# Performance work log

Hardware: AMD Instinct MI355X
Metric: run time of the kernel (lower is better)

The kernel has to match this reference:

```python
import jax, jax.numpy as jnp
import numpy as np
from jax.scipy.linalg import expm
jax.config.update("jax_enable_x64", True)

HBAR = 0.6582119569
CM2EV = 0.00012398419
N6A, N10A = 4, 4
DT = 1.0
KDC = dict(E_S1=3.995, E_S2=4.9183, om6a=596.0 * CM2EV, om10a=919.0 * CM2EV,
           kap6a_S1=-0.0964, kap6a_S2=0.1193, lam=0.1825, gamma=-0.018)


def _build():
    cd = np.complex128

    def ladder(n):
        a = np.zeros((n, n), dtype=cd)
        for k in range(1, n):
            a[k - 1, k] = np.sqrt(float(k))
        adag = a.conj().T
        return (a + adag) / np.sqrt(2.0), adag @ a, np.eye(n, dtype=cd)

    Q6a1, N6a1, I6a = ladder(N6A)
    Q10a1, N10a1, I10a = ladder(N10A)
    Nel, Dvib = 3, N6A * N10A
    Ivib = np.eye(Dvib, dtype=cd)
    Iel = np.eye(Nel, dtype=cd)
    lift = lambda op: np.kron(Iel, op)
    Q6a = lift(np.kron(Q6a1, I10a))
    Q10a = lift(np.kron(I6a, Q10a1))
    N6a = lift(np.kron(N6a1, I10a))
    N10a = lift(np.kron(I6a, N10a1))
    P = []
    for k in range(Nel):
        ek = np.zeros(Nel, dtype=cd); ek[k] = 1.0
        P.append(np.kron(np.outer(ek, ek), Ivib))
    e1 = np.zeros(Nel, dtype=cd); e1[1] = 1.0
    e2 = np.zeros(Nel, dtype=cd); e2[2] = 1.0
    Poff = np.kron(np.outer(e1, e2) + np.outer(e2, e1), Ivib)
    Lj = np.kron(np.outer(e1, e2), Ivib)  # |S1><S2| lift
    D = Nel * Dvib
    I = np.eye(D, dtype=cd)
    p = KDC
    H = (p['E_S1'] * P[1] + p['E_S2'] * P[2] + p['om6a'] * N6a + p['om10a'] * N10a
         + p['kap6a_S1'] * P[1] @ Q6a + p['kap6a_S2'] * P[2] @ Q6a
         + p['lam'] * Poff @ Q10a + p['gamma'] * Poff @ (Q10a @ Q10a))
    # Coherent part -i(I kron H - H^T* kron I); dissipator at unit rate (scaled by g later)
    Lc = -1j * (np.kron(I, H) - np.kron(H.conj().T, I))
    LdL = Lj.conj().T @ Lj
    Ld0 = (np.kron(Lj.conj(), Lj) - 0.5 * np.kron(I, LdL)
           - 0.5 * np.kron(LdL.conj().T, I))
    psi = np.zeros(D, dtype=cd); psi[2 * N6A * N10A] = 1.0
    rho0 = np.outer(psi, psi.conj()).reshape(-1)
    trP = np.stack([P[k].T.reshape(-1) for k in range(3)])  # [3, D^2]
    return Lc, Ld0, rho0, trP

_LC, _LD0, _RHO0, _TRP = _build()


def setup_inputs() -> dict:
    return {"log_g": jnp.asarray(np.log(1.0 / 40.0), dtype=jnp.float32),
            "n_steps": 1000}


def reference(log_g, n_steps):
    Lc = jnp.asarray(_LC)
    Ld0 = jnp.asarray(_LD0)
    rho0 = jnp.asarray(_RHO0)
    trP = jnp.asarray(_TRP)
    g = jnp.exp(log_g).astype(jnp.float64)
    Lsup = Lc + g * Ld0                      # [D^2, D^2] complex128
    U = expm(Lsup * (DT / HBAR))             # one-step propagator

    def step(rho, _):
        pops = jnp.real(trP @ rho)           # tr(P_k rho), k=0..2
        return U @ rho, pops

    _, ps = jax.lax.scan(step, rho0, None, length=int(n_steps))  # [n_steps, 3]
    return (ps[:, 0].astype(jnp.float32),
            ps[:, 1].astype(jnp.float32),
            ps[:, 2].astype(jnp.float32))
```

## Files before the change

kernel.cpp:

```cpp
#include <hip/hip_runtime.h>
#include <math.h>


#define DS 1024
#define MATD ((size_t)DS * DS * sizeof(double))
#define PA 66

typedef double v4d __attribute__((ext_vector_type(4)));

__device__ inline double Qel(int i, int j) {
    if (i == j + 1) return sqrt((double)i) * 0.70710678118654752440;
    if (j == i + 1) return sqrt((double)j) * 0.70710678118654752440;
    return 0.0;
}

__device__ inline void fill_H(double* Hs, int tid) {
    const double CM2EV = 0.00012398419;
    const double E_S1 = 3.995, E_S2 = 4.9183;
    const double om6a = 596.0 * CM2EV, om10a = 919.0 * CM2EV;
    const double kapA = -0.0964, kapB = 0.1193, lam = 0.1825, gam = -0.018;
    for (int h = tid; h < 1024; h += 256) {
        int r = h >> 5, c = h & 31;
        int e = r >> 4, v6 = (r >> 2) & 3, v10 = r & 3;
        int e2 = c >> 4, w6 = (c >> 2) & 3, w10 = c & 3;
        double val = 0.0;
        if (r == c) val += (e ? E_S2 : E_S1) + om6a * v6 + om10a * v10;
        if (e == e2 && v10 == w10) val += (e ? kapB : kapA) * Qel(v6, w6);
        if (e != e2 && v6 == w6) {
            double q2 = 0.0;
            #pragma unroll
            for (int m = 0; m < 4; ++m) q2 += Qel(v10, m) * Qel(m, w10);
            val += lam * Qel(v10, w10) + gam * q2;
        }
        Hs[h] = val;
    }
}

__global__ __launch_bounds__(256)
void build_G14(const float* __restrict__ logg, double* __restrict__ X,
               double* __restrict__ Y, double* __restrict__ Z)
{
    int tid = threadIdx.x;
    if (blockIdx.x >= 4096) {
        int idx = (blockIdx.x - 4096) * 256 + tid;
        if (idx < 64 * 1024) {
            int r = idx >> 10, i = idx & 1023;
            double v = 0.0;
            if (r < 2 && i % 33 == 0) {
                int a = i / 33;
                if ((a < 16) == (r == 0)) v = 1.0;
            }
            Y[idx] = v;
        } else if (idx < 64 * 1024 + 1024) {
            int i = idx - 64 * 1024;
            Z[i] = (i == 528) ? 1.0 : 0.0;
        }
        return;
    }
    __shared__ double Hs[1024];
    fill_H(Hs, tid);
    __syncthreads();
    double g = exp((double)logg[0]);
    const double sc = ((1.0 / 0.6582119569) / 8.0) / 14.0;
    int idx = blockIdx.x * 256 + tid;
    int r = idx >> 10, c = idx & 1023;
    int i = r >> 5, j = r & 31;
    int k = c >> 5, l = c & 31;
    double t = 0.0;
    if (k <= l) {
        if (i <= j) {
            if (i < 16 && j < 16) {
                int p = i + 16, q = j + 16;
                if ((p == k && q == l) || (p == l && q == k)) t += g;
            }
            if (i == k && j == l) t -= 0.5 * g * ((i >= 16) + (j >= 16));
        } else {
            if (j == l) t += Hs[i * 32 + k];
            if (k != l && j == k) t += Hs[i * 32 + l];
            if (i == k) t -= Hs[l * 32 + j];
            if (k != l && i == l) t -= Hs[k * 32 + j];
        }
    } else {
        if (i <= j) {
            double ha = 0.0;
            if (j == l) ha += Hs[i * 32 + k];
            if (j == k) ha -= Hs[i * 32 + l];
            if (i == k) ha -= Hs[l * 32 + j];
            if (i == l) ha += Hs[k * 32 + j];
            t -= ha;
        } else {
            if (i < 16 && j < 16 && (i + 16 == k) && (j + 16 == l)) t += g;
            if (i == k && j == l) t -= 0.5 * g * ((i >= 16) + (j >= 16));
        }
    }
    X[idx] = t * sc + ((r == c) ? 1.0 : 0.0);
}

__global__ __launch_bounds__(256)
void apply_T(const float* __restrict__ logg, const double* __restrict__ M,
             double* __restrict__ O, double invk)
{
    __shared__ double Hs[1024];
    const int tid = threadIdx.x;
    fill_H(Hs, tid);
    __syncthreads();
    const double g = exp((double)logg[0]);
    const double sck = ((1.0 / 0.6582119569) / 8.0) * invk;
    const int p = ((blockIdx.x & 7) << 7) | (blockIdx.x >> 3);
    const int i = p >> 5, j = p & 31;

    double a0 = 0.0, a1 = 0.0, a2 = 0.0, a3 = 0.0;
    const int e = tid;

#define ADDROW(q, wgt) { const double* r_ = M + (size_t)(q) * DS; double w_ = (wgt); \
    a0 += w_ * r_[e]; a1 += w_ * r_[e + 256];                                        \
    a2 += w_ * r_[e + 512]; a3 += w_ * r_[e + 768]; }

    if (i <= j) {
        for (int m = 0; m < 32; ++m) {
            double c = Hs[i * 32 + m];
            if (c != 0.0 && m != j) {
                if (m > j) ADDROW(m * 32 + j, -c)
                else       ADDROW(j * 32 + m,  c)
            }
        }
        for (int m = 0; m < 32; ++m) {
            double c = Hs[m * 32 + j];
            if (c != 0.0 && m != i) {
                if (i > m) ADDROW(i * 32 + m,  c)
                else       ADDROW(m * 32 + i, -c)
            }
        }
        if (i < 16 && j < 16) ADDROW((i + 16) * 32 + (j + 16), g)
        if (i >= 16 || j >= 16)
            ADDROW(p, -0.5 * g * (double)((i >= 16) + (j >= 16)))
    } else {
        for (int m = 0; m < 32; ++m) {
            double c = Hs[i * 32 + m];
            if (c != 0.0) {
                int lo = m < j ? m : j, hi = m < j ? j : m;
                ADDROW(lo * 32 + hi, c)
            }
        }
        for (int m = 0; m < 32; ++m) {
            double c = Hs[m * 32 + j];
            if (c != 0.0) {
                int lo = m < i ? m : i, hi = m < i ? i : m;
                ADDROW(lo * 32 + hi, -c)
            }
        }
        if (i < 16 && j < 16) ADDROW((i + 16) * 32 + (j + 16), g)
        ADDROW(p, -0.5 * g * (double)((i >= 16) + (j >= 16)))
    }
#undef ADDROW

    size_t base = (size_t)p * DS;
    O[base + e]       = sck * a0 + ((p == e)       ? 1.0 : 0.0);
    O[base + e + 256] = sck * a1 + ((p == e + 256) ? 1.0 : 0.0);
    O[base + e + 512] = sck * a2 + ((p == e + 512) ? 1.0 : 0.0);
    O[base + e + 768] = sck * a3 + ((p == e + 768) ? 1.0 : 0.0);
}

__global__ __launch_bounds__(1024, 1)
void dgemm(const double* __restrict__ A, const double* __restrict__ B,
           double* __restrict__ D)
{
    __shared__ double As[2][64 * PA];
    __shared__ double Bs[2][64 * PA];
    const int tid = threadIdx.x;
    const int bm = blockIdx.x << 6, bn = blockIdx.y << 6;
    const int w = tid >> 6, lane = tid & 63;
    const int lr = lane & 15, lk = lane >> 4;
    const int p = w & 3, kg = w >> 2;
    const int wr = (p >> 1) << 5, wc = (p & 1) << 5;

    v4d acc[2][2];
    #pragma unroll
    for (int si = 0; si < 2; ++si)
        #pragma unroll
        for (int sj = 0; sj < 2; ++sj) acc[si][sj] = (v4d){0., 0., 0., 0.};

    const int ra = tid >> 4;
    const int cs = (tid & 15) << 2;
    const double* gA = A + (size_t)(bm + ra) * DS + cs;
    const double* gB = B + (size_t)ra * DS + bn + cs;
    double va[4], vb[4];
    #pragma unroll
    for (int u = 0; u < 4; ++u) { va[u] = gA[u]; vb[u] = gB[u]; }
    #pragma unroll
    for (int u = 0; u < 4; ++u) {
        As[0][ra * PA + cs + u] = va[u];
        Bs[0][ra * PA + cs + u] = vb[u];
    }
    __syncthreads();

    #pragma unroll 2
    for (int kt = 0; kt < DS; kt += 64) {
        const int pb = (kt >> 6) & 1;
        const bool more = (kt + 64) < DS;
        if (more) {
            #pragma unroll
            for (int u = 0; u < 4; ++u) {
                va[u] = gA[kt + 64 + u];
                vb[u] = gB[(size_t)(kt + 64) * DS + u];
            }
        }
        const int k0 = (kg << 4) + lk;
        double A00 = As[pb][(wr + lr) * PA + k0];
        double A10 = As[pb][(wr + 16 + lr) * PA + k0];
        double B00 = Bs[pb][k0 * PA + wc + lr];
        double B10 = Bs[pb][k0 * PA + wc + 16 + lr];
        double A01 = As[pb][(wr + lr) * PA + k0 + 4];
        double A11 = As[pb][(wr + 16 + lr) * PA + k0 + 4];
        double B01 = Bs[pb][(k0 + 4) * PA + wc + lr];
        double B11 = Bs[pb][(k0 + 4) * PA + wc + 16 + lr];
        acc[0][0] = __builtin_amdgcn_mfma_f64_16x16x4f64(A00, B00, acc[0][0], 0, 0, 0);
        acc[0][1] = __builtin_amdgcn_mfma_f64_16x16x4f64(A00, B10, acc[0][1], 0, 0, 0);
        acc[1][0] = __builtin_amdgcn_mfma_f64_16x16x4f64(A10, B00, acc[1][0], 0, 0, 0);
        acc[1][1] = __builtin_amdgcn_mfma_f64_16x16x4f64(A10, B10, acc[1][1], 0, 0, 0);
        acc[0][0] = __builtin_amdgcn_mfma_f64_16x16x4f64(A01, B01, acc[0][0], 0, 0, 0);
        acc[0][1] = __builtin_amdgcn_mfma_f64_16x16x4f64(A01, B11, acc[0][1], 0, 0, 0);
        acc[1][0] = __builtin_amdgcn_mfma_f64_16x16x4f64(A11, B01, acc[1][0], 0, 0, 0);
        acc[1][1] = __builtin_amdgcn_mfma_f64_16x16x4f64(A11, B11, acc[1][1], 0, 0, 0);
        if (more) {
            #pragma unroll
            for (int u = 0; u < 4; ++u) {
                As[pb ^ 1][ra * PA + cs + u] = va[u];
                Bs[pb ^ 1][ra * PA + cs + u] = vb[u];
            }
        }
        double A02 = As[pb][(wr + lr) * PA + k0 + 8];
        double A12 = As[pb][(wr + 16 + lr) * PA + k0 + 8];
        double B02 = Bs[pb][(k0 + 8) * PA + wc + lr];
        double B12 = Bs[pb][(k0 + 8) * PA + wc + 16 + lr];
        double A03 = As[pb][(wr + lr) * PA + k0 + 12];
        double A13 = As[pb][(wr + 16 + lr) * PA + k0 + 12];
        double B03 = Bs[pb][(k0 + 12) * PA + wc + lr];
        double B13 = Bs[pb][(k0 + 12) * PA + wc + 16 + lr];
        acc[0][0] = __builtin_amdgcn_mfma_f64_16x16x4f64(A02, B02, acc[0][0], 0, 0, 0);
        acc[0][1] = __builtin_amdgcn_mfma_f64_16x16x4f64(A02, B12, acc[0][1], 0, 0, 0);
        acc[1][0] = __builtin_amdgcn_mfma_f64_16x16x4f64(A12, B02, acc[1][0], 0, 0, 0);
        acc[1][1] = __builtin_amdgcn_mfma_f64_16x16x4f64(A12, B12, acc[1][1], 0, 0, 0);
        acc[0][0] = __builtin_amdgcn_mfma_f64_16x16x4f64(A03, B03, acc[0][0], 0, 0, 0);
        acc[0][1] = __builtin_amdgcn_mfma_f64_16x16x4f64(A03, B13, acc[0][1], 0, 0, 0);
        acc[1][0] = __builtin_amdgcn_mfma_f64_16x16x4f64(A13, B03, acc[1][0], 0, 0, 0);
        acc[1][1] = __builtin_amdgcn_mfma_f64_16x16x4f64(A13, B13, acc[1][1], 0, 0, 0);
        __syncthreads();
    }

    double* red = &As[0][0];
    if (kg == 3) {
        #pragma unroll
        for (int si = 0; si < 2; ++si)
            #pragma unroll
            for (int sj = 0; sj < 2; ++sj)
                #pragma unroll
                for (int r = 0; r < 4; ++r)
                    red[(wr + si * 16 + lk + 4 * r) * 64 + wc + sj * 16 + lr]
                        = acc[si][sj][r];
    }
    __syncthreads();
    if (kg == 2) {
        #pragma unroll
        for (int si = 0; si < 2; ++si)
            #pragma unroll
            for (int sj = 0; sj < 2; ++sj)
                #pragma unroll
                for (int r = 0; r < 4; ++r)
                    red[(wr + si * 16 + lk + 4 * r) * 64 + wc + sj * 16 + lr]
                        += acc[si][sj][r];
    }
    __syncthreads();
    if (kg == 1) {
        #pragma unroll
        for (int si = 0; si < 2; ++si)
            #pragma unroll
            for (int sj = 0; sj < 2; ++sj)
                #pragma unroll
                for (int r = 0; r < 4; ++r)
                    red[(wr + si * 16 + lk + 4 * r) * 64 + wc + sj * 16 + lr]
                        += acc[si][sj][r];
    }
    __syncthreads();
    if (kg == 0) {
        #pragma unroll
        for (int si = 0; si < 2; ++si)
            #pragma unroll
            for (int sj = 0; sj < 2; ++sj) {
                int col = bn + wc + sj * 16 + lr;
                #pragma unroll
                for (int r = 0; r < 4; ++r) {
                    int row = bm + wr + si * 16 + lk + 4 * r;
                    D[(size_t)row * DS + col] = acc[si][sj][r]
                        + red[(wr + si * 16 + lk + 4 * r) * 64 + wc + sj * 16 + lr];
                }
            }
    }
}

__global__ __launch_bounds__(256)
void ypart(const double* __restrict__ P, const double* __restrict__ Y,
           double* __restrict__ scratch, int SR)
{
    __shared__ double Yld[32 * 64];
    __shared__ double red[32 * 64];
    const int tid = threadIdx.x;
    const int cc = tid & 63, kw = tid >> 6;
    const int col = (blockIdx.x << 6) + cc;
    const int kb = blockIdx.y << 6;
    const int r0 = blockIdx.z << 5;

    for (int idx = tid; idx < 32 * 64; idx += 256) {
        int r = idx >> 6, kk = idx & 63;
        Yld[idx] = Y[(size_t)(r0 + r) * DS + kb + kk];
    }
    __syncthreads();

    double acc[32];
    #pragma unroll
    for (int r = 0; r < 32; ++r) acc[r] = 0.0;

    #pragma unroll
    for (int kk = 0; kk < 16; ++kk) {
        int kl = (kw << 4) + kk;
        double pv = P[(size_t)(kb + kl) * DS + col];
        #pragma unroll
        for (int r = 0; r < 32; ++r)
            acc[r] += Yld[(r << 6) + kl] * pv;
    }

    __syncthreads();
    if (kw == 3) {
        #pragma unroll
        for (int r = 0; r < 32; ++r) red[(r << 6) + cc] = acc[r];
    }
    __syncthreads();
    if (kw == 2) {
        #pragma unroll
        for (int r = 0; r < 32; ++r) red[(r << 6) + cc] += acc[r];
    }
    __syncthreads();
    if (kw == 1) {
        #pragma unroll
        for (int r = 0; r < 32; ++r) red[(r << 6) + cc] += acc[r];
    }
    __syncthreads();
    if (kw == 0) {
        #pragma unroll
        for (int r = 0; r < 32; ++r) red[(r << 6) + cc] += acc[r];
    }
    __syncthreads();
    for (int idx = tid; idx < 32 * 64; idx += 256) {
        int r = idx >> 6, c2 = idx & 63;
        scratch[((size_t)blockIdx.y * SR + r0 + r) * DS + (blockIdx.x << 6) + c2]
            = red[idx];
    }
}

__global__ __launch_bounds__(256)
void yreduce(const double* __restrict__ scratch, double* __restrict__ Y,
             int M, int SR)
{
    int idx = blockIdx.x * 256 + threadIdx.x;
    int r = idx >> 10, c = idx & 1023;
    double s = 0.0;
    #pragma unroll
    for (int q = 0; q < 16; ++q)
        s += scratch[((size_t)q * SR + r) * DS + c];
    Y[(size_t)(M + r) * DS + c] = s;
}

__global__ __launch_bounds__(256)
void zstep(const double* __restrict__ V, const double* __restrict__ Zin,
           double* __restrict__ Zout)
{
    int row = blockIdx.x * 4 + (threadIdx.x >> 6);
    int lane = threadIdx.x & 63;
    const double2* r_ = (const double2*)(V + (size_t)row * DS);
    const double2* z_ = (const double2*)Zin;
    double s = 0.0;
    #pragma unroll
    for (int k = 0; k < 8; ++k) {
        double2 a = r_[(k << 6) + lane];
        double2 b = z_[(k << 6) + lane];
        s += a.x * b.x + a.y * b.y;
    }
    #pragma unroll
    for (int off = 32; off; off >>= 1) s += __shfl_down(s, off);
    if (lane == 0) Zout[row] = s;
}

__global__ __launch_bounds__(128)
void final_pops(const double* __restrict__ Y, const double* __restrict__ Z,
                float* __restrict__ out, int n)
{
    int t = blockIdx.x;
    int k = threadIdx.x >> 6, lane = threadIdx.x & 63;
    int a = t & 31, j = t >> 5;
    const double* y = Y + (size_t)(2 * a + k) * 1024;
    const double* z = Z + (size_t)j * 1024;
    double s = 0.0;
    for (int i = lane; i < 1024; i += 64) s += y[i] * z[i];
    #pragma unroll
    for (int off = 32; off; off >>= 1) s += __shfl_down(s, off);
    if (lane == 0) {
        out[(size_t)(k + 1) * n + t] = (float)s;
        if (k == 0) out[t] = 0.0f;
    }
}

static inline void ydouble2(const double* P, double* Y, double* scr, int M,
                            hipStream_t stream)
{
    int gz = (M + 31) / 32; if (gz < 1) gz = 1;
    int SR = gz * 32;
    ypart<<<dim3(16, 16, gz), 256, 0, stream>>>(P, Y, scr, SR);
    yreduce<<<SR * 4, 256, 0, stream>>>(scr, Y, M, SR);
}

extern "C" void kernel_launch(void* const* d_in, const int* in_sizes, int n_in,
                              void* d_out, int out_size, void* d_ws, size_t ws_size,
                              hipStream_t stream)
{
    const float* logg = (const float*)d_in[0];
    float* out = (float*)d_out;
    const int n = out_size / 3;
    (void)in_sizes; (void)n_in; (void)ws_size;

    char* ws = (char*)d_ws;
    double* b0 = (double*)(ws + 0 * MATD);
    double* b1 = (double*)(ws + 1 * MATD);
    double* b2 = (double*)(ws + 2 * MATD);
    double* scr = (double*)(ws + 3 * MATD);
    double* Y  = (double*)(ws + 5 * MATD);
    double* Z  = Y + 64 * 1024;

    dim3 g2(16, 16);

    build_G14<<<4096 + 260, 256, 0, stream>>>(logg, b0, Y, Z);
    double* src = b0; double* dst = b1;
    for (int k = 13; k >= 1; --k) {
        apply_T<<<1024, 256, 0, stream>>>(logg, src, dst, 1.0 / (double)k);
        double* t = src; src = dst; dst = t;
    }

    dgemm<<<g2, 1024, 0, stream>>>(b1, b1, b0);
    dgemm<<<g2, 1024, 0, stream>>>(b0, b0, b2);
    dgemm<<<g2, 1024, 0, stream>>>(b2, b2, b0);
    ydouble2(b0, Y, scr, 2, stream);
    dgemm<<<g2, 1024, 0, stream>>>(b0, b0, b1);
    ydouble2(b1, Y, scr, 4, stream);
    dgemm<<<g2, 1024, 0, stream>>>(b1, b1, b2);
    ydouble2(b2, Y, scr, 8, stream);
    dgemm<<<g2, 1024, 0, stream>>>(b2, b2, b1);
    ydouble2(b1, Y, scr, 16, stream);
    dgemm<<<g2, 1024, 0, stream>>>(b1, b1, b2);
    ydouble2(b2, Y, scr, 32, stream);
    dgemm<<<g2, 1024, 0, stream>>>(b2, b2, b1);

    for (int j = 1; j < 32; ++j)
        zstep<<<256, 256, 0, stream>>>(b1, Z + (size_t)(j - 1) * 1024,
                                       Z + (size_t)j * 1024);

    final_pops<<<n, 128, 0, stream>>>(Y, Z, out, n);
}
```

Before: 689.0 us.

## Retile DGEMM to 64x32 blocks and rebalance expm Taylor order versus squarings

The DGEMM now uses 512-thread blocks computing 64x32 output tiles with a 32-wide K step, and the launch bounds are changed to allow several blocks per CU. The grid doubles to 512 blocks, so all compute units can be busy instead of 256 large blocks. Separately, the matrix-exponential scaling goes from dividing by 8 with a degree-14 Taylor series to dividing by 16 with degree 10, which removes four apply_T passes but adds one extra squaring GEMM. The lower Taylor degree on a smaller-norm matrix may change accuracy slightly, and the smaller tiles give less data reuse per block.

```diff
diff --git a/kernel.cpp b/kernel.cpp
--- a/kernel.cpp
+++ b/kernel.cpp
@@ -4,7 +4,7 @@
 
 #define DS 1024
 #define MATD ((size_t)DS * DS * sizeof(double))
-#define PA 66
+#define PAK 33
 
 typedef double v4d __attribute__((ext_vector_type(4)));
 
@@ -37,7 +37,7 @@
 }
 
 __global__ __launch_bounds__(256)
-void build_G14(const float* __restrict__ logg, double* __restrict__ X,
+void build_G10(const float* __restrict__ logg, double* __restrict__ X,
                double* __restrict__ Y, double* __restrict__ Z)
 {
     int tid = threadIdx.x;
@@ -61,7 +61,7 @@
     fill_H(Hs, tid);
     __syncthreads();
     double g = exp((double)logg[0]);
-    const double sc = ((1.0 / 0.6582119569) / 8.0) / 14.0;
+    const double sc = ((1.0 / 0.6582119569) / 16.0) / 10.0;
     int idx = blockIdx.x * 256 + tid;
     int r = idx >> 10, c = idx & 1023;
     int i = r >> 5, j = r & 31;
@@ -105,7 +105,7 @@
     fill_H(Hs, tid);
     __syncthreads();
     const double g = exp((double)logg[0]);
-    const double sck = ((1.0 / 0.6582119569) / 8.0) * invk;
+    const double sck = ((1.0 / 0.6582119569) / 16.0) * invk;
     const int p = ((blockIdx.x & 7) << 7) | (blockIdx.x >> 3);
     const int i = p >> 5, j = p & 31;
 
@@ -161,18 +161,18 @@
     O[base + e + 768] = sck * a3 + ((p == e + 768) ? 1.0 : 0.0);
 }
 
-__global__ __launch_bounds__(1024, 1)
+__global__ __launch_bounds__(512, 4)
 void dgemm(const double* __restrict__ A, const double* __restrict__ B,
            double* __restrict__ D)
 {
-    __shared__ double As[2][64 * PA];
-    __shared__ double Bs[2][64 * PA];
+    __shared__ double As[2][64 * PAK];
+    __shared__ double Bs[2][32 * PAK];
     const int tid = threadIdx.x;
-    const int bm = blockIdx.x << 6, bn = blockIdx.y << 6;
+    const int bm = blockIdx.x << 6, bn = blockIdx.y << 5;
     const int w = tid >> 6, lane = tid & 63;
     const int lr = lane & 15, lk = lane >> 4;
-    const int p = w & 3, kg = w >> 2;
-    const int wr = (p >> 1) << 5, wc = (p & 1) << 5;
+    const int wp = w & 1, kg = w >> 1;
+    const int wr = wp << 5;
 
     v4d acc[2][2];
     #pragma unroll
@@ -180,71 +180,57 @@
         #pragma unroll
         for (int sj = 0; sj < 2; ++sj) acc[si][sj] = (v4d){0., 0., 0., 0.};
 
-    const int ra = tid >> 4;
-    const int cs = (tid & 15) << 2;
-    const double* gA = A + (size_t)(bm + ra) * DS + cs;
-    const double* gB = B + (size_t)ra * DS + bn + cs;
-    double va[4], vb[4];
-    #pragma unroll
-    for (int u = 0; u < 4; ++u) { va[u] = gA[u]; vb[u] = gB[u]; }
-    #pragma unroll
-    for (int u = 0; u < 4; ++u) {
-        As[0][ra * PA + cs + u] = va[u];
-        Bs[0][ra * PA + cs + u] = vb[u];
-    }
+    const int arow = tid >> 3, acol = (tid & 7) << 2;
+    const int brow = tid >> 4, bcol = (tid & 15) << 1;
+    const double* gA = A + (size_t)(bm + arow) * DS + acol;
+    const double* gB = B + (size_t)brow * DS + bn + bcol;
+    double va[4], vb[2];
+    #pragma unroll
+    for (int u = 0; u < 4; ++u) va[u] = gA[u];
+    #pragma unroll
+    for (int u = 0; u < 2; ++u) vb[u] = gB[u];
+    #pragma unroll
+    for (int u = 0; u < 4; ++u) As[0][arow * PAK + acol + u] = va[u];
+    #pragma unroll
+    for (int u = 0; u < 2; ++u) Bs[0][brow * PAK + bcol + u] = vb[u];
     __syncthreads();
 
     #pragma unroll 2
-    for (int kt = 0; kt < DS; kt += 64) {
-        const int pb = (kt >> 6) & 1;
-        const bool more = (kt + 64) < DS;
+    for (int kt = 0; kt < DS; kt += 32) {
+        const int pb = (kt >> 5) & 1;
+        const bool more = (kt + 32) < DS;
         if (more) {
             #pragma unroll
-            for (int u = 0; u < 4; ++u) {
-                va[u] = gA[kt + 64 + u];
-                vb[u] = gB[(size_t)(kt + 64) * DS + u];
-            }
-        }
-        const int k0 = (kg << 4) + lk;
-        double A00 = As[pb][(wr + lr) * PA + k0];
-        double A10 = As[pb][(wr + 16 + lr) * PA + k0];
-        double B00 = Bs[pb][k0 * PA + wc + lr];
-        double B10 = Bs[pb][k0 * PA + wc + 16 + lr];
-        double A01 = As[pb][(wr + lr) * PA + k0 + 4];
-        double A11 = As[pb][(wr + 16 + lr) * PA + k0 + 4];
-        double B01 = Bs[pb][(k0 + 4) * PA + wc + lr];
-        double B11 = Bs[pb][(k0 + 4) * PA + wc + 16 + lr];
+            for (int u = 0; u < 4; ++u) va[u] = gA[kt + 32 + u];
+            #pragma unroll
+            for (int u = 0; u < 2; ++u)
+                vb[u] = gB[(size_t)(kt + 32) * DS + u];
+        }
+        const int k0 = (kg << 3) + lk;
+        double A00 = As[pb][(wr + lr) * PAK + k0];
+        double A10 = As[pb][(wr + 16 + lr) * PAK + k0];
+        double B00 = Bs[pb][k0 * PAK + lr];
+        double B10 = Bs[pb][k0 * PAK + 16 + lr];
         acc[0][0] = __builtin_amdgcn_mfma_f64_16x16x4f64(A00, B00, acc[0][0], 0, 0, 0);
         acc[0][1] = __builtin_amdgcn_mfma_f64_16x16x4f64(A00, B10, acc[0][1], 0, 0, 0);
         acc[1][0] = __builtin_amdgcn_mfma_f64_16x16x4f64(A10, B00, acc[1][0], 0, 0, 0);
         acc[1][1] = __builtin_amdgcn_mfma_f64_16x16x4f64(A10, B10, acc[1][1], 0, 0, 0);
+        if (more) {
+            #pragma unroll
+            for (int u = 0; u < 4; ++u)
+                As[pb ^ 1][arow * PAK + acol + u] = va[u];
+            #pragma unroll
+            for (int u = 0; u < 2; ++u)
+                Bs[pb ^ 1][brow * PAK + bcol + u] = vb[u];
+        }
+        double A01 = As[pb][(wr + lr) * PAK + k0 + 4];
+        double A11 = As[pb][(wr + 16 + lr) * PAK + k0 + 4];
+        double B01 = Bs[pb][(k0 + 4) * PAK + lr];
+        double B11 = Bs[pb][(k0 + 4) * PAK + 16 + lr];
         acc[0][0] = __builtin_amdgcn_mfma_f64_16x16x4f64(A01, B01, acc[0][0], 0, 0, 0);
         acc[0][1] = __builtin_amdgcn_mfma_f64_16x16x4f64(A01, B11, acc[0][1], 0, 0, 0);
         acc[1][0] = __builtin_amdgcn_mfma_f64_16x16x4f64(A11, B01, acc[1][0], 0, 0, 0);
         acc[1][1] = __builtin_amdgcn_mfma_f64_16x16x4f64(A11, B11, acc[1][1], 0, 0, 0);
-        if (more) {
-            #pragma unroll
-            for (int u = 0; u < 4; ++u) {
-                As[pb ^ 1][ra * PA + cs + u] = va[u];
-                Bs[pb ^ 1][ra * PA + cs + u] = vb[u];
-            }
-        }
-        double A02 = As[pb][(wr + lr) * PA + k0 + 8];
-        double A12 = As[pb][(wr + 16 + lr) * PA + k0 + 8];
-        double B02 = Bs[pb][(k0 + 8) * PA + wc + lr];
-        double B12 = Bs[pb][(k0 + 8) * PA + wc + 16 + lr];
-        double A03 = As[pb][(wr + lr) * PA + k0 + 12];
-        double A13 = As[pb][(wr + 16 + lr) * PA + k0 + 12];
-        double B03 = Bs[pb][(k0 + 12) * PA + wc + lr];
-        double B13 = Bs[pb][(k0 + 12) * PA + wc + 16 + lr];
-        acc[0][0] = __builtin_amdgcn_mfma_f64_16x16x4f64(A02, B02, acc[0][0], 0, 0, 0);
-        acc[0][1] = __builtin_amdgcn_mfma_f64_16x16x4f64(A02, B12, acc[0][1], 0, 0, 0);
-        acc[1][0] = __builtin_amdgcn_mfma_f64_16x16x4f64(A12, B02, acc[1][0], 0, 0, 0);
-        acc[1][1] = __builtin_amdgcn_mfma_f64_16x16x4f64(A12, B12, acc[1][1], 0, 0, 0);
-        acc[0][0] = __builtin_amdgcn_mfma_f64_16x16x4f64(A03, B03, acc[0][0], 0, 0, 0);
-        acc[0][1] = __builtin_amdgcn_mfma_f64_16x16x4f64(A03, B13, acc[0][1], 0, 0, 0);
-        acc[1][0] = __builtin_amdgcn_mfma_f64_16x16x4f64(A13, B03, acc[1][0], 0, 0, 0);
-        acc[1][1] = __builtin_amdgcn_mfma_f64_16x16x4f64(A13, B13, acc[1][1], 0, 0, 0);
         __syncthreads();
     }
 
@@ -256,7 +242,7 @@
             for (int sj = 0; sj < 2; ++sj)
                 #pragma unroll
                 for (int r = 0; r < 4; ++r)
-                    red[(wr + si * 16 + lk + 4 * r) * 64 + wc + sj * 16 + lr]
+                    red[(wr + si * 16 + lk + 4 * r) * 32 + sj * 16 + lr]
                         = acc[si][sj][r];
     }
     __syncthreads();
@@ -267,7 +253,7 @@
             for (int sj = 0; sj < 2; ++sj)
                 #pragma unroll
                 for (int r = 0; r < 4; ++r)
-                    red[(wr + si * 16 + lk + 4 * r) * 64 + wc + sj * 16 + lr]
+                    red[(wr + si * 16 + lk + 4 * r) * 32 + sj * 16 + lr]
                         += acc[si][sj][r];
     }
     __syncthreads();
@@ -278,7 +264,7 @@
             for (int sj = 0; sj < 2; ++sj)
                 #pragma unroll
                 for (int r = 0; r < 4; ++r)
-                    red[(wr + si * 16 + lk + 4 * r) * 64 + wc + sj * 16 + lr]
+                    red[(wr + si * 16 + lk + 4 * r) * 32 + sj * 16 + lr]
                         += acc[si][sj][r];
     }
     __syncthreads();
@@ -287,12 +273,12 @@
         for (int si = 0; si < 2; ++si)
             #pragma unroll
             for (int sj = 0; sj < 2; ++sj) {
-                int col = bn + wc + sj * 16 + lr;
+                int col = bn + sj * 16 + lr;
                 #pragma unroll
                 for (int r = 0; r < 4; ++r) {
                     int row = bm + wr + si * 16 + lk + 4 * r;
                     D[(size_t)row * DS + col] = acc[si][sj][r]
-                        + red[(wr + si * 16 + lk + 4 * r) * 64 + wc + sj * 16 + lr];
+                        + red[(wr + si * 16 + lk + 4 * r) * 32 + sj * 16 + lr];
                 }
             }
     }
@@ -435,28 +421,29 @@
     double* Y  = (double*)(ws + 5 * MATD);
     double* Z  = Y + 64 * 1024;
 
-    dim3 g2(16, 16);
-
-    build_G14<<<4096 + 260, 256, 0, stream>>>(logg, b0, Y, Z);
+    dim3 gg(16, 32);
+
+    build_G10<<<4096 + 260, 256, 0, stream>>>(logg, b0, Y, Z);
     double* src = b0; double* dst = b1;
-    for (int k = 13; k >= 1; --k) {
+    for (int k = 9; k >= 1; --k) {
         apply_T<<<1024, 256, 0, stream>>>(logg, src, dst, 1.0 / (double)k);
         double* t = src; src = dst; dst = t;
     }
 
-    dgemm<<<g2, 1024, 0, stream>>>(b1, b1, b0);
-    dgemm<<<g2, 1024, 0, stream>>>(b0, b0, b2);
-    dgemm<<<g2, 1024, 0, stream>>>(b2, b2, b0);
+    dgemm<<<gg, 512, 0, stream>>>(b1, b1, b0);
+    dgemm<<<gg, 512, 0, stream>>>(b0, b0, b2);
+    dgemm<<<gg, 512, 0, stream>>>(b2, b2, b1);
+    dgemm<<<gg, 512, 0, stream>>>(b1, b1, b0);
     ydouble2(b0, Y, scr, 2, stream);
-    dgemm<<<g2, 1024, 0, stream>>>(b0, b0, b1);
+    dgemm<<<gg, 512, 0, stream>>>(b0, b0, b1);
     ydouble2(b1, Y, scr, 4, stream);
-    dgemm<<<g2, 1024, 0, stream>>>(b1, b1, b2);
+    dgemm<<<gg, 512, 0, stream>>>(b1, b1, b2);
     ydouble2(b2, Y, scr, 8, stream);
-    dgemm<<<g2, 1024, 0, stream>>>(b2, b2, b1);
+    dgemm<<<gg, 512, 0, stream>>>(b2, b2, b1);
     ydouble2(b1, Y, scr, 16, stream);
-    dgemm<<<g2, 1024, 0, stream>>>(b1, b1, b2);
+    dgemm<<<gg, 512, 0, stream>>>(b1, b1, b2);
     ydouble2(b2, Y, scr, 32, stream);
-    dgemm<<<g2, 1024, 0, stream>>>(b2, b2, b1);
+    dgemm<<<gg, 512, 0, stream>>>(b2, b2, b1);
 
     for (int j = 1; j < 32; ++j)
         zstep<<<256, 256, 0, stream>>>(b1, Z + (size_t)(j - 1) * 1024,
```

Result: no change. 686.3 us (-0.4%).

## Rebalance expm: degree-10 Taylor with extra squaring, compact apply_T row list

Applied to the files above, without the earlier changes.

The matrix exponential now uses a scaling of 1/16 instead of 1/8, with a degree-10 Taylor polynomial instead of degree 14. That drops four sparse apply_T passes and adds one dense 1024x1024 DGEMM squaring. apply_T now builds a compacted list of nonzero row indices and weights in shared memory with a ballot, then runs a uniform unrolled loop with double2 loads instead of branchy per-row loops. The lower Taylor degree on a smaller-norm argument could change accuracy slightly.

```diff
diff --git a/kernel.cpp b/kernel.cpp
--- a/kernel.cpp
+++ b/kernel.cpp
@@ -37,7 +37,7 @@
 }
 
 __global__ __launch_bounds__(256)
-void build_G14(const float* __restrict__ logg, double* __restrict__ X,
+void build_G10(const float* __restrict__ logg, double* __restrict__ X,
                double* __restrict__ Y, double* __restrict__ Z)
 {
     int tid = threadIdx.x;
@@ -61,7 +61,7 @@
     fill_H(Hs, tid);
     __syncthreads();
     double g = exp((double)logg[0]);
-    const double sc = ((1.0 / 0.6582119569) / 8.0) / 14.0;
+    const double sc = ((1.0 / 0.6582119569) / 16.0) / 10.0;
     int idx = blockIdx.x * 256 + tid;
     int r = idx >> 10, c = idx & 1023;
     int i = r >> 5, j = r & 31;
@@ -101,64 +101,80 @@
              double* __restrict__ O, double invk)
 {
     __shared__ double Hs[1024];
+    __shared__ double wlist[72];
+    __shared__ int    qlist[72];
+    __shared__ int    Kshared;
     const int tid = threadIdx.x;
     fill_H(Hs, tid);
     __syncthreads();
     const double g = exp((double)logg[0]);
-    const double sck = ((1.0 / 0.6582119569) / 8.0) * invk;
+    const double sck = ((1.0 / 0.6582119569) / 16.0) * invk;
     const int p = ((blockIdx.x & 7) << 7) | (blockIdx.x >> 3);
     const int i = p >> 5, j = p & 31;
 
+    if (tid < 64) {
+        const int m = tid & 31;
+        const bool loop2 = tid >= 32;
+        double c = loop2 ? Hs[m * 32 + j] : Hs[i * 32 + m];
+        int q = 0; double w = 0.0; bool valid;
+        if (i <= j) {
+            if (!loop2) {
+                valid = (c != 0.0) && (m != j);
+                q = (m > j) ? m * 32 + j : j * 32 + m;
+                w = (m > j) ? -c : c;
+            } else {
+                valid = (c != 0.0) && (m != i);
+                q = (i > m) ? i * 32 + m : m * 32 + i;
+                w = (i > m) ? c : -c;
+            }
+        } else {
+            if (!loop2) {
+                valid = (c != 0.0);
+                int lo = m < j ? m : j, hi = m < j ? j : m;
+                q = lo * 32 + hi; w = c;
+            } else {
+                valid = (c != 0.0);
+                int lo = m < i ? m : i, hi = m < i ? i : m;
+                q = lo * 32 + hi; w = -c;
+            }
+        }
+        unsigned long long mask = __ballot(valid);
+        int slot = __popcll(mask & ((1ull << tid) - 1ull));
+        if (valid) { qlist[slot] = q; wlist[slot] = w; }
+        if (tid == 0) {
+            int K = __popcll(mask);
+            if (i < 16 && j < 16) {
+                qlist[K] = (i + 16) * 32 + (j + 16); wlist[K] = g; ++K;
+            }
+            double wd = -0.5 * g * (double)((i >= 16) + (j >= 16));
+            if (wd != 0.0) { qlist[K] = p; wlist[K] = wd; ++K; }
+            while (K & 3) { qlist[K] = 0; wlist[K] = 0.0; ++K; }
+            Kshared = K;
+        }
+    }
+    __syncthreads();
+    const int K = Kshared;
+
     double a0 = 0.0, a1 = 0.0, a2 = 0.0, a3 = 0.0;
-    const int e = tid;
-
-#define ADDROW(q, wgt) { const double* r_ = M + (size_t)(q) * DS; double w_ = (wgt); \
-    a0 += w_ * r_[e]; a1 += w_ * r_[e + 256];                                        \
-    a2 += w_ * r_[e + 512]; a3 += w_ * r_[e + 768]; }
-
-    if (i <= j) {
-        for (int m = 0; m < 32; ++m) {
-            double c = Hs[i * 32 + m];
-            if (c != 0.0 && m != j) {
-                if (m > j) ADDROW(m * 32 + j, -c)
-                else       ADDROW(j * 32 + m,  c)
-            }
-        }
-        for (int m = 0; m < 32; ++m) {
-            double c = Hs[m * 32 + j];
-            if (c != 0.0 && m != i) {
-                if (i > m) ADDROW(i * 32 + m,  c)
-                else       ADDROW(m * 32 + i, -c)
-            }
-        }
-        if (i < 16 && j < 16) ADDROW((i + 16) * 32 + (j + 16), g)
-        if (i >= 16 || j >= 16)
-            ADDROW(p, -0.5 * g * (double)((i >= 16) + (j >= 16)))
-    } else {
-        for (int m = 0; m < 32; ++m) {
-            double c = Hs[i * 32 + m];
-            if (c != 0.0) {
-                int lo = m < j ? m : j, hi = m < j ? j : m;
-                ADDROW(lo * 32 + hi, c)
-            }
-        }
-        for (int m = 0; m < 32; ++m) {
-            double c = Hs[m * 32 + j];
-            if (c != 0.0) {
-                int lo = m < i ? m : i, hi = m < i ? i : m;
-                ADDROW(lo * 32 + hi, -c)
-            }
-        }
-        if (i < 16 && j < 16) ADDROW((i + 16) * 32 + (j + 16), g)
-        ADDROW(p, -0.5 * g * (double)((i >= 16) + (j >= 16)))
-    }
-#undef ADDROW
-
-    size_t base = (size_t)p * DS;
-    O[base + e]       = sck * a0 + ((p == e)       ? 1.0 : 0.0);
-    O[base + e + 256] = sck * a1 + ((p == e + 256) ? 1.0 : 0.0);
-    O[base + e + 512] = sck * a2 + ((p == e + 512) ? 1.0 : 0.0);
-    O[base + e + 768] = sck * a3 + ((p == e + 768) ? 1.0 : 0.0);
+    const double2* Mp = (const double2*)M;
+    const int e2 = tid << 1;
+    for (int k = 0; k < K; k += 4) {
+        #pragma unroll
+        for (int u = 0; u < 4; ++u) {
+            int q = qlist[k + u];
+            double w = wlist[k + u];
+            double2 v0 = Mp[(size_t)q * (DS / 2) + e2];
+            double2 v1 = Mp[(size_t)q * (DS / 2) + e2 + 1];
+            a0 += w * v0.x; a1 += w * v0.y;
+            a2 += w * v1.x; a3 += w * v1.y;
+        }
+    }
+    const int c0 = tid << 2;
+    size_t base = (size_t)p * DS + c0;
+    O[base + 0] = sck * a0 + ((p == c0)     ? 1.0 : 0.0);
+    O[base + 1] = sck * a1 + ((p == c0 + 1) ? 1.0 : 0.0);
+    O[base + 2] = sck * a2 + ((p == c0 + 2) ? 1.0 : 0.0);
+    O[base + 3] = sck * a3 + ((p == c0 + 3) ? 1.0 : 0.0);
 }
 
 __global__ __launch_bounds__(1024, 1)
@@ -437,16 +453,17 @@
 
     dim3 g2(16, 16);
 
-    build_G14<<<4096 + 260, 256, 0, stream>>>(logg, b0, Y, Z);
+    build_G10<<<4096 + 260, 256, 0, stream>>>(logg, b0, Y, Z);
     double* src = b0; double* dst = b1;
-    for (int k = 13; k >= 1; --k) {
+    for (int k = 9; k >= 1; --k) {
         apply_T<<<1024, 256, 0, stream>>>(logg, src, dst, 1.0 / (double)k);
         double* t = src; src = dst; dst = t;
     }
 
     dgemm<<<g2, 1024, 0, stream>>>(b1, b1, b0);
     dgemm<<<g2, 1024, 0, stream>>>(b0, b0, b2);
-    dgemm<<<g2, 1024, 0, stream>>>(b2, b2, b0);
+    dgemm<<<g2, 1024, 0, stream>>>(b2, b2, b1);
+    dgemm<<<g2, 1024, 0, stream>>>(b1, b1, b0);
     ydouble2(b0, Y, scr, 2, stream);
     dgemm<<<g2, 1024, 0, stream>>>(b0, b0, b1);
     ydouble2(b1, Y, scr, 4, stream);
```

After: 653.5 us. -5.2%, faster.
